# Kernel optimization log

Hardware: AMD Instinct MI355X
Metric: run time of the kernel (lower is better)

## Reference

```python
import jax, jax.numpy as jnp
import numpy as np
from jax import lax

R = 7                      # pooler_resolution
SCALES = (0.25, 0.125, 0.0625, 0.03125)
SCORE_THRESH = 0.05        # args.roi_test_score_thresh
NMS_THRESH = 0.5           # args.roi_nms_thresh
TOPK = 100                 # args.roi_nms_topk_post
SCALE_CLAMP = float(np.log(1000.0 / 16))


def _pool_level(f, boxes, scale):
    # f: [C,H,W]; boxes: [M,4] in image coords. RoIPool approximated by
    # nearest-neighbor sample at each of the 7x7 bin centers.
    C, H, W = f.shape
    b = boxes * scale
    x1, y1, x2, y2 = b[:, 0], b[:, 1], b[:, 2], b[:, 3]
    bw = jnp.maximum(x2 - x1, 1.0) / R
    bh = jnp.maximum(y2 - y1, 1.0) / R
    cs = jnp.arange(R, dtype=b.dtype) + 0.5
    gx = x1[:, None] + cs * bw[:, None]          # [M,R]
    gy = y1[:, None] + cs * bh[:, None]          # [M,R]
    ix = jnp.clip(gx.astype(jnp.int32), 0, W - 1)
    iy = jnp.clip(gy.astype(jnp.int32), 0, H - 1)
    fh = jnp.transpose(f, (1, 2, 0))             # [H,W,C]
    out = fh[iy[:, :, None], ix[:, None, :]]     # [M,R,R,C]
    return jnp.transpose(out, (0, 3, 1, 2))      # [M,C,R,R]


def _assign_levels(boxes):
    # detectron2-style FPN level assignment: canonical level 4 at size 224
    w = boxes[:, 2] - boxes[:, 0]
    h = boxes[:, 3] - boxes[:, 1]
    s = jnp.sqrt(jnp.maximum(w * h, 1e-6))
    lvl = jnp.floor(4.0 + jnp.log2(s / 224.0 + 1e-8))
    return jnp.clip(lvl, 2, 5).astype(jnp.int32) - 2   # index into p2..p5


def _pool_image(f2, f3, f4, f5, boxes):
    pooled = jnp.stack([_pool_level(f, boxes, s)
                        for f, s in zip((f2, f3, f4, f5), SCALES)])  # [4,M,C,R,R]
    idx = _assign_levels(boxes)
    return pooled[idx, jnp.arange(boxes.shape[0])]     # [M,C,R,R]


def _apply_deltas(boxes, deltas):
    w = boxes[:, 2] - boxes[:, 0]
    h = boxes[:, 3] - boxes[:, 1]
    cx = boxes[:, 0] + 0.5 * w
    cy = boxes[:, 1] + 0.5 * h
    dx, dy = deltas[:, 0], deltas[:, 1]
    dw = jnp.minimum(deltas[:, 2], SCALE_CLAMP)
    dh = jnp.minimum(deltas[:, 3], SCALE_CLAMP)
    pcx = dx * w + cx
    pcy = dy * h + cy
    pw = jnp.exp(dw) * w
    ph = jnp.exp(dh) * h
    return jnp.stack([pcx - 0.5 * pw, pcy - 0.5 * ph,
                      pcx + 0.5 * pw, pcy + 0.5 * ph], axis=1)


def _pairwise_iou(a, b):
    area_a = (a[:, 2] - a[:, 0]) * (a[:, 3] - a[:, 1])
    area_b = (b[:, 2] - b[:, 0]) * (b[:, 3] - b[:, 1])
    lt = jnp.maximum(a[:, None, :2], b[None, :, :2])
    rb = jnp.minimum(a[:, None, 2:], b[None, :, 2:])
    wh = jnp.clip(rb - lt, 0.0)
    inter = wh[..., 0] * wh[..., 1]
    return inter / jnp.maximum(area_a[:, None] + area_b[None, :] - inter, 1e-9)


def _nms_image(boxes, scores, hw):
    # boxes [M,4], scores [M], hw = (H,W) float
    H, W = hw[0], hw[1]
    boxes = jnp.stack([jnp.clip(boxes[:, 0], 0.0, W),
                       jnp.clip(boxes[:, 1], 0.0, H),
                       jnp.clip(boxes[:, 2], 0.0, W),
                       jnp.clip(boxes[:, 3], 0.0, H)], axis=1)
    order = jnp.argsort(-scores)
    b = boxes[order]
    s = scores[order]
    M = b.shape[0]
    keep0 = s > SCORE_THRESH
    iou = _pairwise_iou(b, b)
    idx = jnp.arange(M)

    def body(i, keep):
        suppress = (iou[i] > NMS_THRESH) & (idx > i) & keep[i]
        return keep & ~suppress

    keep = lax.fori_loop(0, M, body, keep0)
    keep = keep & (jnp.cumsum(keep.astype(jnp.int32)) <= TOPK)
    return b, s, keep, order


def setup_inputs() -> dict:
    key = jax.random.key(0)
    ks = jax.random.split(key, 12)
    N, M, C = 2, 1000, 256
    H, W = 800, 1216
    fc_in, fc_dim = C * R * R, 1024
    p2 = jax.random.normal(ks[0], (N, C, H // 4, W // 4), jnp.float32)
    p3 = jax.random.normal(ks[1], (N, C, H // 8, W // 8), jnp.float32)
    p4 = jax.random.normal(ks[2], (N, C, H // 16, W // 16), jnp.float32)
    p5 = jax.random.normal(ks[3], (N, C, H // 32, W // 32), jnp.float32)
    u = jax.random.uniform(ks[4], (N, M, 4))
    cx = u[..., 0] * (W - 1)
    cy = u[..., 1] * (H - 1)
    bw = 16.0 + u[..., 2] * 480.0
    bh = 16.0 + u[..., 3] * 480.0
    x1 = jnp.clip(cx - 0.5 * bw, 0.0, W - 8.0)
    y1 = jnp.clip(cy - 0.5 * bh, 0.0, H - 8.0)
    x2 = jnp.clip(cx + 0.5 * bw, x1 + 4.0, float(W))
    y2 = jnp.clip(cy + 0.5 * bh, y1 + 4.0, float(H))
    proposals = jnp.stack([x1, y1, x2, y2], axis=-1)
    image_sizes = jnp.array([[H, W], [H, W]], dtype=jnp.int32)
    return {
        'p2': p2, 'p3': p3, 'p4': p4, 'p5': p5,
        'proposals': proposals, 'image_sizes': image_sizes,
        'W1': jax.random.normal(ks[5], (fc_in, fc_dim), jnp.float32) * 0.01,
        'b1': jnp.zeros((fc_dim,), jnp.float32),
        'W2': jax.random.normal(ks[6], (fc_dim, fc_dim), jnp.float32) * 0.01,
        'b2': jnp.zeros((fc_dim,), jnp.float32),
        'Wc': jax.random.normal(ks[7], (fc_dim, 2), jnp.float32) * 0.01,
        'bc': jnp.zeros((2,), jnp.float32),
        'Wb': jax.random.normal(ks[8], (fc_dim, 4), jnp.float32) * 0.001,
        'bb': jnp.zeros((4,), jnp.float32),
    }


def reference(p2, p3, p4, p5, proposals, image_sizes,
              W1, b1, W2, b2, Wc, bc, Wb, bb):
    N, M, _ = proposals.shape
    pooled = jax.vmap(_pool_image)(p2, p3, p4, p5, proposals)  # [N,M,C,R,R]
    x = pooled.reshape(N * M, -1)
    x = jax.nn.relu(x @ W1 + b1)
    x = jax.nn.relu(x @ W2 + b2)
    cls_score = x @ Wc + bc                                    # [NM,2]
    deltas = x @ Wb + bb                                       # [NM,4]
    scores = jax.nn.softmax(cls_score, axis=1)[:, 1].reshape(N, M)
    pred_boxes = _apply_deltas(proposals.reshape(-1, 4), deltas).reshape(N, M, 4)
    boxes_s, scores_s, keep, order = jax.vmap(_nms_image)(
        pred_boxes, scores, image_sizes.astype(jnp.float32))
    return boxes_s, scores_s, keep, order
```

## Files before the change

kernel.cpp:

```cpp
#include <hip/hip_runtime.h>
#include <math.h>

#define NBOX 1000
#define NIMG 2
#define CCH 256
#define FCIN 12544
#define FCD 1024
#define TOPK 100
#define SCALE_CLAMP_F ((float)4.135166556742356)
#define KC 384
#define NPANEL 33
#define RB 16
#define NGROUP 125
#define R1 8

__global__ void prep_kernel(const float* __restrict__ props, int* __restrict__ prep) {
    int b = blockIdx.x * blockDim.x + threadIdx.x;
    if (b >= NIMG * NBOX) return;
    int n = b / NBOX;
    const float* pr = props + (size_t)b * 4;
    float x1 = pr[0], y1 = pr[1], x2 = pr[2], y2 = pr[3];

    float w = __fsub_rn(x2, x1), h = __fsub_rn(y2, y1);
    float s = sqrtf(fmaxf(__fmul_rn(w, h), 1e-6f));
    float l2 = (float)log2((double)__fadd_rn(__fdiv_rn(s, 224.0f), 1e-8f));
    float lv = floorf(__fadd_rn(4.0f, l2));
    lv = fminf(fmaxf(lv, 2.0f), 5.0f);
    int lvl = (int)lv - 2;

    int H, W; float scale;
    if (lvl == 0)      { H = 200; W = 304; scale = 0.25f; }
    else if (lvl == 1) { H = 100; W = 152; scale = 0.125f; }
    else if (lvl == 2) { H = 50;  W = 76;  scale = 0.0625f; }
    else               { H = 25;  W = 38;  scale = 0.03125f; }

    float xs1 = __fmul_rn(x1, scale), ys1 = __fmul_rn(y1, scale);
    float xs2 = __fmul_rn(x2, scale), ys2 = __fmul_rn(y2, scale);
    float bw = __fdiv_rn(fmaxf(__fsub_rn(xs2, xs1), 1.0f), 7.0f);
    float bh = __fdiv_rn(fmaxf(__fsub_rn(ys2, ys1), 1.0f), 7.0f);

    int* pb = prep + b * 20;
    pb[0] = lvl;
    pb[1] = n * CCH * H * W;
    pb[2] = H * W;
#pragma unroll
    for (int i = 0; i < 7; i++) {
        float cs = (float)i + 0.5f;
        float gx = __fadd_rn(xs1, __fmul_rn(cs, bw));
        float gy = __fadd_rn(ys1, __fmul_rn(cs, bh));
        int vx = (int)gx;
        int vy = (int)gy;
        vx = vx < 0 ? 0 : (vx > W - 1 ? W - 1 : vx);
        vy = vy < 0 ? 0 : (vy > H - 1 ? H - 1 : vy);
        pb[4 + i] = vx;
        pb[12 + i] = vy * W;
    }
}

#define LOAD8(DST, Q)                                  \
    {                                                  \
        float4 t0 = *(const float4*)(Q);               \
        float4 t1 = *(const float4*)((Q) + 4);         \
        DST[0] = t0.x; DST[1] = t0.y; DST[2] = t0.z; DST[3] = t0.w; \
        DST[4] = t1.x; DST[5] = t1.y; DST[6] = t1.z; DST[7] = t1.w; \
    }

#define FMABLK(KB, WBUF)                                              \
    {                                                                 \
        const float4* xv = (const float4*)&xs[(KB)][0];               \
        float4 a0 = xv[0], a1 = xv[1], a2 = xv[2], a3 = xv[3];        \
        float xr[16] = {a0.x, a0.y, a0.z, a0.w, a1.x, a1.y, a1.z, a1.w, \
                        a2.x, a2.y, a2.z, a2.w, a3.x, a3.y, a3.z, a3.w}; \
        _Pragma("unroll")                                             \
        for (int r = 0; r < RB; r++) {                                \
            _Pragma("unroll")                                         \
            for (int j = 0; j < 8; j++)                               \
                acc[r][j] = fmaf(xr[r], WBUF[j], acc[r][j]);          \
        }                                                             \
    }

template <int KT>
__global__ __launch_bounds__(128, 2) void fc1_panel(
    const float* __restrict__ p2, const float* __restrict__ p3,
    const float* __restrict__ p4, const float* __restrict__ p5,
    const int* __restrict__ prep, const float* __restrict__ W1,
    float* __restrict__ part, int g0, int gs, int p_base) {
    __shared__ float xs[KT][RB];
    __shared__ int s_ix[RB][7], s_iyW[RB][7], s_HW[RB];
    __shared__ const float* s_fp[RB];

    int tid = threadIdx.x;
    int gy = blockIdx.x;
    int p = p_base + blockIdx.y;
    int row0 = (g0 + gy) * RB;
    int k0 = p * KC;

    if (tid < RB) {
        const int* pb = prep + (row0 + tid) * 20;
        int lvl = pb[0];
        s_fp[tid] = (lvl == 0 ? p2 : lvl == 1 ? p3 : lvl == 2 ? p4 : p5) + pb[1];
        s_HW[tid] = pb[2];
#pragma unroll
        for (int j = 0; j < 7; j++) { s_ix[tid][j] = pb[4 + j]; s_iyW[tid][j] = pb[12 + j]; }
    }
    __syncthreads();

    for (int e = tid; e < KT * RB; e += 128) {
        int kk = e >> 4;
        int r = e & 15;
        int k = k0 + kk;
        int c = k / 49;
        int pp = k - c * 49;
        int gyy = pp / 7;
        int gxx = pp - gyy * 7;
        xs[kk][r] = s_fp[r][c * s_HW[r] + s_iyW[r][gyy] + s_ix[r][gxx]];
    }
    __syncthreads();

    float acc[RB][8];
#pragma unroll
    for (int r = 0; r < RB; r++)
#pragma unroll
        for (int j = 0; j < 8; j++) acc[r][j] = 0.0f;

    const float* wp = W1 + (size_t)k0 * FCD + tid * 8;
    float wA[8], wB[8];
    LOAD8(wA, wp)
    for (int kk = 0; kk < KT; kk += 2) {
        LOAD8(wB, wp + (size_t)(kk + 1) * FCD)
        FMABLK(kk, wA)
        if (kk + 2 < KT) LOAD8(wA, wp + (size_t)(kk + 2) * FCD)
        FMABLK(kk + 1, wB)
    }

    size_t pstride = (size_t)gs * RB * FCD;
    float* po = part + (size_t)p * pstride + ((size_t)gy * RB) * FCD + tid * 8;
#pragma unroll
    for (int r = 0; r < RB; r++) {
#pragma unroll
        for (int j = 0; j < 8; j++) po[(size_t)r * FCD + j] = acc[r][j];
    }
}

__global__ void fc1_fold(const float* __restrict__ part, const float* __restrict__ b1,
                         float* __restrict__ X1, int row_base, int rows_s) {
    int idx = blockIdx.x * 256 + threadIdx.x;
    if (idx >= rows_s * FCD) return;
    size_t stride = (size_t)rows_s * FCD;
    float tot = part[idx];
    for (int p = 1; p < NPANEL; p++)
        tot = __fadd_rn(tot, part[(size_t)p * stride + idx]);
    int c = idx & (FCD - 1);
    float v = __fadd_rn(tot, b1[c]);
    X1[(size_t)row_base * FCD + idx] = fmaxf(v, 0.0f);
}

#define FMA8(BUF, KB)                                                                   \
    _Pragma("unroll")                                                                   \
    for (int u = 0; u < 8; u++) {                                                       \
        const float4* xv = (const float4*)&xs[(KB) + u][0];                             \
        float4 a0 = xv[0], a1 = xv[1];                                                  \
        float wx = BUF[u].x, wy = BUF[u].y;                                             \
        acc[0][0] = fmaf(a0.x, wx, acc[0][0]); acc[0][1] = fmaf(a0.x, wy, acc[0][1]);   \
        acc[1][0] = fmaf(a0.y, wx, acc[1][0]); acc[1][1] = fmaf(a0.y, wy, acc[1][1]);   \
        acc[2][0] = fmaf(a0.z, wx, acc[2][0]); acc[2][1] = fmaf(a0.z, wy, acc[2][1]);   \
        acc[3][0] = fmaf(a0.w, wx, acc[3][0]); acc[3][1] = fmaf(a0.w, wy, acc[3][1]);   \
        acc[4][0] = fmaf(a1.x, wx, acc[4][0]); acc[4][1] = fmaf(a1.x, wy, acc[4][1]);   \
        acc[5][0] = fmaf(a1.y, wx, acc[5][0]); acc[5][1] = fmaf(a1.y, wy, acc[5][1]);   \
        acc[6][0] = fmaf(a1.z, wx, acc[6][0]); acc[6][1] = fmaf(a1.z, wy, acc[6][1]);   \
        acc[7][0] = fmaf(a1.w, wx, acc[7][0]); acc[7][1] = fmaf(a1.w, wy, acc[7][1]);   \
    }

template <int KT>
__device__ __forceinline__ void fc_panel2(const float* __restrict__ wp,
                                          const float (*xs)[R1],
                                          float acc[R1][2]) {
    float2 wa[8], wb[8];
#pragma unroll
    for (int u = 0; u < 8; u++) wa[u] = *(const float2*)(wp + (size_t)u * FCD);
    for (int kk = 0; kk < KT; kk += 16) {
#pragma unroll
        for (int u = 0; u < 8; u++)
            wb[u] = *(const float2*)(wp + (size_t)(kk + 8 + u) * FCD);
        FMA8(wa, kk)
        if (kk + 16 < KT) {
#pragma unroll
            for (int u = 0; u < 8; u++)
                wa[u] = *(const float2*)(wp + (size_t)(kk + 16 + u) * FCD);
        }
        FMA8(wb, kk + 8)
    }
}

__global__ __launch_bounds__(256) void fc1_fallback(
    const float* __restrict__ p2, const float* __restrict__ p3,
    const float* __restrict__ p4, const float* __restrict__ p5,
    const int* __restrict__ prep, const float* __restrict__ W1,
    const float* __restrict__ b1, float* __restrict__ X1) {
    __shared__ float xs[KC][R1];
    __shared__ int s_ix[R1][7], s_iyW[R1][7], s_HW[R1];
    __shared__ const float* s_fp[R1];

    int tid = threadIdx.x;
    int c0 = blockIdx.x * 512 + tid * 2;
    int row0 = blockIdx.y * R1;

    if (tid < R1) {
        const int* pb = prep + (row0 + tid) * 20;
        int lvl = pb[0];
        s_fp[tid] = (lvl == 0 ? p2 : lvl == 1 ? p3 : lvl == 2 ? p4 : p5) + pb[1];
        s_HW[tid] = pb[2];
#pragma unroll
        for (int j = 0; j < 7; j++) { s_ix[tid][j] = pb[4 + j]; s_iyW[tid][j] = pb[12 + j]; }
    }

    float tot[R1][2];
#pragma unroll
    for (int r = 0; r < R1; r++) { tot[r][0] = 0.0f; tot[r][1] = 0.0f; }

    for (int k0 = 0; k0 < FCIN; k0 += KC) {
        int kt = FCIN - k0; if (kt > KC) kt = KC;
        __syncthreads();
        for (int e = tid; e < kt * R1; e += 256) {
            int kk = e >> 3;
            int r = e & 7;
            int k = k0 + kk;
            int c = k / 49;
            int p = k - c * 49;
            int gy = p / 7;
            int gx = p - gy * 7;
            xs[kk][r] = s_fp[r][c * s_HW[r] + s_iyW[r][gy] + s_ix[r][gx]];
        }
        __syncthreads();

        float acc[R1][2];
#pragma unroll
        for (int r = 0; r < R1; r++) { acc[r][0] = 0.0f; acc[r][1] = 0.0f; }

        const float* wp = W1 + (size_t)k0 * FCD + c0;
        if (kt == KC) fc_panel2<KC>(wp, xs, acc);
        else          fc_panel2<256>(wp, xs, acc);

#pragma unroll
        for (int r = 0; r < R1; r++) {
            tot[r][0] = __fadd_rn(tot[r][0], acc[r][0]);
            tot[r][1] = __fadd_rn(tot[r][1], acc[r][1]);
        }
    }
    float bv0 = b1[c0], bv1 = b1[c0 + 1];
#pragma unroll
    for (int r = 0; r < R1; r++) {
        float v0 = __fadd_rn(tot[r][0], bv0);
        float v1 = __fadd_rn(tot[r][1], bv1);
        X1[(size_t)(row0 + r) * FCD + c0]     = fmaxf(v0, 0.0f);
        X1[(size_t)(row0 + r) * FCD + c0 + 1] = fmaxf(v1, 0.0f);
    }
}

__global__ __launch_bounds__(256) void fc2_seq(
    const float* __restrict__ X1, const float* __restrict__ W2,
    const float* __restrict__ b2, float* __restrict__ X2) {
    __shared__ float xs[KC][R1];
    int tid = threadIdx.x;
    int c0 = blockIdx.x * 512 + tid * 2;
    int row0 = blockIdx.y * R1;

    float tot[R1][2];
#pragma unroll
    for (int r = 0; r < R1; r++) { tot[r][0] = 0.0f; tot[r][1] = 0.0f; }

    for (int k0 = 0; k0 < FCD; k0 += KC) {
        int kt = FCD - k0; if (kt > KC) kt = KC;
        __syncthreads();
        for (int e = tid; e < kt * R1; e += 256) {
            int kk = e >> 3;
            int r = e & 7;
            xs[kk][r] = X1[(size_t)(row0 + r) * FCD + k0 + kk];
        }
        __syncthreads();

        float acc[R1][2];
#pragma unroll
        for (int r = 0; r < R1; r++) { acc[r][0] = 0.0f; acc[r][1] = 0.0f; }

        const float* wp = W2 + (size_t)k0 * FCD + c0;
        if (kt == KC) fc_panel2<KC>(wp, xs, acc);
        else          fc_panel2<256>(wp, xs, acc);

#pragma unroll
        for (int r = 0; r < R1; r++) {
            tot[r][0] = __fadd_rn(tot[r][0], acc[r][0]);
            tot[r][1] = __fadd_rn(tot[r][1], acc[r][1]);
        }
    }
    float bv0 = b2[c0], bv1 = b2[c0 + 1];
#pragma unroll
    for (int r = 0; r < R1; r++) {
        float v0 = __fadd_rn(tot[r][0], bv0);
        float v1 = __fadd_rn(tot[r][1], bv1);
        X2[(size_t)(row0 + r) * FCD + c0]     = fmaxf(v0, 0.0f);
        X2[(size_t)(row0 + r) * FCD + c0 + 1] = fmaxf(v1, 0.0f);
    }
}

__global__ __launch_bounds__(256) void heads_seq(
    const float* __restrict__ X2,
    const float* __restrict__ Wc, const float* __restrict__ bc,
    const float* __restrict__ Wb, const float* __restrict__ bb_,
    const float* __restrict__ props, const int* __restrict__ img_sz,
    float* __restrict__ SC, float* __restrict__ BX) {
    int b = blockIdx.x;
    int tid = threadIdx.x;
    __shared__ float xsh[FCD];
    __shared__ float lg[6];
    for (int k = tid; k < FCD; k += 256) xsh[k] = X2[(size_t)b * FCD + k];
    __syncthreads();

    if (tid < 6) {
        const float* wp; int st; float bias;
        if (tid < 2) { wp = Wc + tid; st = 2; bias = bc[tid]; }
        else         { wp = Wb + (tid - 2); st = 4; bias = bb_[tid - 2]; }
        float tot = 0.0f;
        for (int k0 = 0; k0 < FCD; k0 += KC) {
            int kt = FCD - k0; if (kt > KC) kt = KC;
            float acc = 0.0f;
            for (int k = k0; k < k0 + kt; k++) acc = fmaf(xsh[k], wp[(size_t)k * st], acc);
            tot = __fadd_rn(tot, acc);
        }
        lg[tid] = __fadd_rn(tot, bias);
    }
    __syncthreads();

    if (tid == 0) {
        float c0 = lg[0], c1 = lg[1];
        float mx = fmaxf(c0, c1);
        float e0 = (float)exp((double)__fsub_rn(c0, mx));
        float e1 = (float)exp((double)__fsub_rn(c1, mx));
        SC[b] = __fdiv_rn(e1, __fadd_rn(e0, e1));

        int n = b / NBOX;
        const float* pr = props + (size_t)b * 4;
        float x1 = pr[0], y1 = pr[1], x2 = pr[2], y2 = pr[3];
        float w = __fsub_rn(x2, x1), h = __fsub_rn(y2, y1);
        float cx = __fadd_rn(x1, __fmul_rn(0.5f, w));
        float cy = __fadd_rn(y1, __fmul_rn(0.5f, h));
        float dx = lg[2], dy = lg[3];
        float dw = fminf(lg[4], SCALE_CLAMP_F);
        float dh = fminf(lg[5], SCALE_CLAMP_F);
        float pcx = __fadd_rn(__fmul_rn(dx, w), cx);
        float pcy = __fadd_rn(__fmul_rn(dy, h), cy);
        float pw = __fmul_rn((float)exp((double)dw), w);
        float ph = __fmul_rn((float)exp((double)dh), h);
        float bx1 = __fsub_rn(pcx, __fmul_rn(0.5f, pw));
        float by1 = __fsub_rn(pcy, __fmul_rn(0.5f, ph));
        float bx2 = __fadd_rn(pcx, __fmul_rn(0.5f, pw));
        float by2 = __fadd_rn(pcy, __fmul_rn(0.5f, ph));
        float Hf = (float)img_sz[n * 2 + 0], Wf = (float)img_sz[n * 2 + 1];
        bx1 = fminf(fmaxf(bx1, 0.0f), Wf);
        by1 = fminf(fmaxf(by1, 0.0f), Hf);
        bx2 = fminf(fmaxf(bx2, 0.0f), Wf);
        by2 = fminf(fmaxf(by2, 0.0f), Hf);
        BX[(size_t)b * 4 + 0] = bx1;
        BX[(size_t)b * 4 + 1] = by1;
        BX[(size_t)b * 4 + 2] = bx2;
        BX[(size_t)b * 4 + 3] = by2;
    }
}

__global__ __launch_bounds__(1024) void nms_kernel(const float* __restrict__ SC,
                                                   const float* __restrict__ BX,
                                                   float* __restrict__ out) {
    int n = blockIdx.x;
    __shared__ float sraw[NBOX];
    __shared__ float ssort[NBOX];
    __shared__ float bsort[NBOX][4];
    __shared__ int ord[NBOX];
    __shared__ unsigned char keep[NBOX];
    int tid = threadIdx.x;

    for (int j = tid; j < NBOX; j += 1024) sraw[j] = SC[n * NBOX + j];
    __syncthreads();

    if (tid < NBOX) {
        float sj = sraw[tid];
        int r = 0;
        for (int k = 0; k < NBOX; k++) {
            float sk = sraw[k];
            r += (sk > sj) || (sk == sj && k < tid);
        }
        ord[r] = tid;
        ssort[r] = sj;
#pragma unroll
        for (int k = 0; k < 4; k++) bsort[r][k] = BX[((size_t)n * NBOX + tid) * 4 + k];
        keep[r] = (sj > 0.05f) ? 1 : 0;
    }
    __syncthreads();

    for (int i = 0; i < NBOX - 1; i++) {
        if (keep[i] && tid > i && tid < NBOX && keep[tid]) {
            float ax1 = bsort[i][0], ay1 = bsort[i][1], ax2 = bsort[i][2], ay2 = bsort[i][3];
            float bx1 = bsort[tid][0], by1 = bsort[tid][1], bx2 = bsort[tid][2], by2 = bsort[tid][3];
            float areaA = __fmul_rn(__fsub_rn(ax2, ax1), __fsub_rn(ay2, ay1));
            float areaB = __fmul_rn(__fsub_rn(bx2, bx1), __fsub_rn(by2, by1));
            float ix1 = fmaxf(ax1, bx1), iy1 = fmaxf(ay1, by1);
            float ix2 = fminf(ax2, bx2), iy2 = fminf(ay2, by2);
            float iw = fmaxf(__fsub_rn(ix2, ix1), 0.0f);
            float ih = fmaxf(__fsub_rn(iy2, iy1), 0.0f);
            float inter = __fmul_rn(iw, ih);
            float denom = fmaxf(__fsub_rn(__fadd_rn(areaA, areaB), inter), 1e-9f);
            if (__fdiv_rn(inter, denom) > 0.5f) keep[tid] = 0;
        }
        __syncthreads();
    }

    if (tid == 0) {
        int c = 0;
        for (int r = 0; r < NBOX; r++) {
            int k = keep[r];
            c += k;
            keep[r] = (k && (c <= TOPK)) ? 1 : 0;
        }
    }
    __syncthreads();

    float* boxes_o = out;
    float* scores_o = out + (size_t)NIMG * NBOX * 4;
    float* keep_o = scores_o + (size_t)NIMG * NBOX;
    float* ord_o = keep_o + (size_t)NIMG * NBOX;
    for (int r = tid; r < NBOX; r += 1024) {
#pragma unroll
        for (int k = 0; k < 4; k++)
            boxes_o[((size_t)n * NBOX + r) * 4 + k] = bsort[r][k];
        scores_o[n * NBOX + r] = ssort[r];
        keep_o[n * NBOX + r] = (float)keep[r];
        ord_o[n * NBOX + r] = (float)ord[r];
    }
}

extern "C" void kernel_launch(void* const* d_in, const int* in_sizes, int n_in,
                              void* d_out, int out_size, void* d_ws, size_t ws_size,
                              hipStream_t stream) {
    const float* p2 = (const float*)d_in[0];
    const float* p3 = (const float*)d_in[1];
    const float* p4 = (const float*)d_in[2];
    const float* p5 = (const float*)d_in[3];
    const float* props = (const float*)d_in[4];
    const int* img = (const int*)d_in[5];
    const float* W1 = (const float*)d_in[6];
    const float* b1 = (const float*)d_in[7];
    const float* W2 = (const float*)d_in[8];
    const float* b2 = (const float*)d_in[9];
    const float* Wc = (const float*)d_in[10];
    const float* bc = (const float*)d_in[11];
    const float* Wb = (const float*)d_in[12];
    const float* bb = (const float*)d_in[13];

    float* X1 = (float*)d_ws;
    float* X2 = X1 + (size_t)2000 * FCD;
    float* SCf = X2 + (size_t)2000 * FCD;
    float* BXf = SCf + 2000;
    int* prep = (int*)(BXf + 8000);
    float* part = (float*)(prep + 2000 * 20);
    size_t used = (size_t)((char*)part - (char*)d_ws);
    size_t avail = ws_size > used ? ws_size - used : 0;

    prep_kernel<<<(NIMG * NBOX + 255) / 256, 256, 0, stream>>>(props, prep);

    int gmax = 0;
    const int cand[4] = {125, 63, 32, 16};
    for (int i = 0; i < 4; i++) {
        size_t need = (size_t)NPANEL * cand[i] * RB * FCD * sizeof(float);
        if (need <= avail) { gmax = cand[i]; break; }
    }

    if (gmax > 0) {
        for (int g0 = 0; g0 < NGROUP; g0 += gmax) {
            int gs = NGROUP - g0; if (gs > gmax) gs = gmax;
            dim3 gA(gs, NPANEL - 1);
            fc1_panel<KC><<<gA, 128, 0, stream>>>(p2, p3, p4, p5, prep, W1, part, g0, gs, 0);
            dim3 gB(gs, 1);
            fc1_panel<256><<<gB, 128, 0, stream>>>(p2, p3, p4, p5, prep, W1, part, g0, gs, 32);
            int rows_s = gs * RB;
            int nelem = rows_s * FCD;
            fc1_fold<<<(nelem + 255) / 256, 256, 0, stream>>>(part, b1, X1, g0 * RB, rows_s);
        }
    } else {
        dim3 gfc(2, (NIMG * NBOX) / R1);
        fc1_fallback<<<gfc, 256, 0, stream>>>(p2, p3, p4, p5, prep, W1, b1, X1);
    }

    dim3 gfc2(2, (NIMG * NBOX) / R1);
    fc2_seq<<<gfc2, 256, 0, stream>>>(X1, W2, b2, X2);

    heads_seq<<<NIMG * NBOX, 256, 0, stream>>>(X2, Wc, bc, Wb, bb, props, img, SCf, BXf);

    nms_kernel<<<NIMG, 1024, 0, stream>>>(SCf, BXf, (float*)d_out);
}
```

Baseline: 1.326 ms.

## Restructure fc1 panel kernel to 256 threads with 4 columns each and chunked gather

The fc1 panel kernel moves from 128 threads computing 8 output columns each to 256 threads computing 4 columns each. This halves the per-thread accumulator registers and raises the launch bound to 4 blocks per SM, aiming for higher occupancy and better latency hiding. The pooled-input gather into shared memory is now done in 128-row chunks with syncs between them, which cuts LDS use, and the two launches (full panels plus the short tail panel) merge into one with a runtime K length. In exchange, each weight element read is reused across fewer columns per thread, and the per-chunk barriers add synchronisation.

```diff
diff --git a/kernel.cpp b/kernel.cpp
--- a/kernel.cpp
+++ b/kernel.cpp
@@ -12,6 +12,7 @@
 #define NPANEL 33
 #define RB 16
 #define NGROUP 125
+#define CHUNK 128
 #define R1 8
 
 __global__ void prep_kernel(const float* __restrict__ props, int* __restrict__ prep) {
@@ -57,15 +58,7 @@
     }
 }
 
-#define LOAD8(DST, Q)                                  \
-    {                                                  \
-        float4 t0 = *(const float4*)(Q);               \
-        float4 t1 = *(const float4*)((Q) + 4);         \
-        DST[0] = t0.x; DST[1] = t0.y; DST[2] = t0.z; DST[3] = t0.w; \
-        DST[4] = t1.x; DST[5] = t1.y; DST[6] = t1.z; DST[7] = t1.w; \
-    }
-
-#define FMABLK(KB, WBUF)                                              \
+#define FMASTEP(KB, WV)                                               \
     {                                                                 \
         const float4* xv = (const float4*)&xs[(KB)][0];               \
         float4 a0 = xv[0], a1 = xv[1], a2 = xv[2], a3 = xv[3];        \
@@ -73,27 +66,28 @@
                         a2.x, a2.y, a2.z, a2.w, a3.x, a3.y, a3.z, a3.w}; \
         _Pragma("unroll")                                             \
         for (int r = 0; r < RB; r++) {                                \
-            _Pragma("unroll")                                         \
-            for (int j = 0; j < 8; j++)                               \
-                acc[r][j] = fmaf(xr[r], WBUF[j], acc[r][j]);          \
+            acc[r][0] = fmaf(xr[r], WV.x, acc[r][0]);                 \
+            acc[r][1] = fmaf(xr[r], WV.y, acc[r][1]);                 \
+            acc[r][2] = fmaf(xr[r], WV.z, acc[r][2]);                 \
+            acc[r][3] = fmaf(xr[r], WV.w, acc[r][3]);                 \
         }                                                             \
     }
 
-template <int KT>
-__global__ __launch_bounds__(128, 2) void fc1_panel(
+__global__ __launch_bounds__(256, 4) void fc1_panel(
     const float* __restrict__ p2, const float* __restrict__ p3,
     const float* __restrict__ p4, const float* __restrict__ p5,
     const int* __restrict__ prep, const float* __restrict__ W1,
-    float* __restrict__ part, int g0, int gs, int p_base) {
-    __shared__ float xs[KT][RB];
+    float* __restrict__ part, int g0, int gs) {
+    __shared__ float xs[CHUNK][RB];
     __shared__ int s_ix[RB][7], s_iyW[RB][7], s_HW[RB];
     __shared__ const float* s_fp[RB];
 
     int tid = threadIdx.x;
     int gy = blockIdx.x;
-    int p = p_base + blockIdx.y;
+    int p = blockIdx.y;
     int row0 = (g0 + gy) * RB;
     int k0 = p * KC;
+    int kt = (p == NPANEL - 1) ? 256 : KC;
 
     if (tid < RB) {
         const int* pb = prep + (row0 + tid) * 20;
@@ -105,40 +99,44 @@
     }
     __syncthreads();
 
-    for (int e = tid; e < KT * RB; e += 128) {
-        int kk = e >> 4;
-        int r = e & 15;
-        int k = k0 + kk;
-        int c = k / 49;
-        int pp = k - c * 49;
-        int gyy = pp / 7;
-        int gxx = pp - gyy * 7;
-        xs[kk][r] = s_fp[r][c * s_HW[r] + s_iyW[r][gyy] + s_ix[r][gxx]];
-    }
-    __syncthreads();
-
-    float acc[RB][8];
+    float acc[RB][4];
 #pragma unroll
     for (int r = 0; r < RB; r++)
 #pragma unroll
-        for (int j = 0; j < 8; j++) acc[r][j] = 0.0f;
-
-    const float* wp = W1 + (size_t)k0 * FCD + tid * 8;
-    float wA[8], wB[8];
-    LOAD8(wA, wp)
-    for (int kk = 0; kk < KT; kk += 2) {
-        LOAD8(wB, wp + (size_t)(kk + 1) * FCD)
-        FMABLK(kk, wA)
-        if (kk + 2 < KT) LOAD8(wA, wp + (size_t)(kk + 2) * FCD)
-        FMABLK(kk + 1, wB)
+        for (int j = 0; j < 4; j++) acc[r][j] = 0.0f;
+
+    const float* wp = W1 + (size_t)k0 * FCD + tid * 4;
+
+    for (int ck = 0; ck < kt; ck += CHUNK) {
+        for (int e = tid; e < CHUNK * RB; e += 256) {
+            int kk = e >> 4;
+            int r = e & 15;
+            int k = k0 + ck + kk;
+            int c = k / 49;
+            int pp = k - c * 49;
+            int gyy = pp / 7;
+            int gxx = pp - gyy * 7;
+            xs[kk][r] = s_fp[r][c * s_HW[r] + s_iyW[r][gyy] + s_ix[r][gxx]];
+        }
+        __syncthreads();
+
+        const float* wc = wp + (size_t)ck * FCD;
+        float4 wA = *(const float4*)wc;
+        for (int kk = 0; kk < CHUNK; kk += 2) {
+            float4 wB = *(const float4*)(wc + (size_t)(kk + 1) * FCD);
+            FMASTEP(kk, wA)
+            if (kk + 2 < CHUNK) wA = *(const float4*)(wc + (size_t)(kk + 2) * FCD);
+            FMASTEP(kk + 1, wB)
+        }
+        __syncthreads();
     }
 
     size_t pstride = (size_t)gs * RB * FCD;
-    float* po = part + (size_t)p * pstride + ((size_t)gy * RB) * FCD + tid * 8;
+    float* po = part + (size_t)p * pstride + ((size_t)gy * RB) * FCD + tid * 4;
 #pragma unroll
     for (int r = 0; r < RB; r++) {
-#pragma unroll
-        for (int j = 0; j < 8; j++) po[(size_t)r * FCD + j] = acc[r][j];
+        float4 v = make_float4(acc[r][0], acc[r][1], acc[r][2], acc[r][3]);
+        *(float4*)(po + (size_t)r * FCD) = v;
     }
 }
 
@@ -476,10 +474,8 @@
     if (gmax > 0) {
         for (int g0 = 0; g0 < NGROUP; g0 += gmax) {
             int gs = NGROUP - g0; if (gs > gmax) gs = gmax;
-            dim3 gA(gs, NPANEL - 1);
-            fc1_panel<KC><<<gA, 128, 0, stream>>>(p2, p3, p4, p5, prep, W1, part, g0, gs, 0);
-            dim3 gB(gs, 1);
-            fc1_panel<256><<<gB, 128, 0, stream>>>(p2, p3, p4, p5, prep, W1, part, g0, gs, 32);
+            dim3 gA(gs, NPANEL);
+            fc1_panel<<<gA, 256, 0, stream>>>(p2, p3, p4, p5, prep, W1, part, g0, gs);
             int rows_s = gs * RB;
             int nelem = rows_s * FCD;
             fc1_fold<<<(nelem + 255) / 256, 256, 0, stream>>>(part, b1, X1, g0 * RB, rows_s);
```

Result: faster. 1.177 ms (-11.2%).
